# Kernel tuning notes

Measured on AMD Instinct MI355X. Metric: run time of the kernel, lower is better.

## Reference

```python
import jax, jax.numpy as jnp
import numpy as np


def _flip(x, c):
    # reflection about index c along the last (W) axis: out[..., i] = x[..., (c - i) mod W]
    W = x.shape[-1]
    idx = (c - jnp.arange(W)) % W
    return x[..., idx]


def setup_inputs() -> dict:
    key = jax.random.key(0)
    k1, k2, k3 = jax.random.split(key, 3)
    B, C, H, W = 8, 32, 256, 256
    x = jax.random.normal(k1, (B, C, H, W), dtype=jnp.float32)
    s = jax.random.normal(k2, (B, 11), dtype=jnp.float32)
    w = jax.random.uniform(k3, (B, 1, H, W), dtype=jnp.float32)
    w_param = jnp.ones((1,), dtype=jnp.float32)
    b_param = jnp.zeros((1,), dtype=jnp.float32)
    return {"x": x, "s": s, "w": w, "w_param": w_param, "b_param": b_param}


def reference(x, s, w, w_param, b_param):
    B, C, H, W = x.shape
    step = W // 8  # 32 for W=256
    # s -> sigmoid(w*s + b), shape [B, 11, 1, 1]
    sg = jax.nn.sigmoid(w_param * s + b_param).reshape(B, -1, 1, 1)
    # 7 circular shifts (45..315 deg) + 4 reflections
    a = w * x
    b = w
    for i in range(7):  # shifts step*1 .. step*7, gated by sg[:, 0..6]
        n = step * (i + 1)
        wk = sg[:, i:i + 1] * jnp.roll(w, n, axis=3)
        a = a + wk * jnp.roll(x, n, axis=3)
        b = b + wk
    for j in range(4):  # flips about step*1-1 .. step*4-1, gated by sg[:, 7..10]
        c = step * (j + 1) - 1
        wk = sg[:, 7 + j:8 + j] * _flip(w, c)
        a = a + wk * _flip(x, c)
        b = b + wk
    return a / b
```

## Files before the change

### kernel.cpp

```cpp
#include <hip/hip_runtime.h>
#include <math.h>

#define BB 8
#define CC 32
#define HH 256
#define WW 256
#define CHW (CC * HH * WW)
#define HW  (HH * WW)
#define NTERM 12
#define CH_PER_ITER 4

__global__ __launch_bounds__(256)
void symctrl2_kernel(const float* __restrict__ x,
                     const float* __restrict__ s,
                     const float* __restrict__ w,
                     const float* __restrict__ w_param,
                     const float* __restrict__ b_param,
                     float* __restrict__ out) {
    const int bh = blockIdx.x;
    const int b  = bh >> 8;
    const int h  = bh & (HH - 1);
    const int i  = threadIdx.x;

    __shared__ float w_row[WW];
    __shared__ float sg[11];
    __shared__ float x_lds[CH_PER_ITER][WW];

    const float* wrow_g = w + ((size_t)b * HH + h) * WW;
    w_row[i] = wrow_g[i];

    if (i < 11) {
        float v = w_param[0] * s[b * 11 + i] + b_param[0];
        sg[i] = 1.0f / (1.0f + expf(-v));
    }
    __syncthreads();

    int   src[NTERM];
    float gw[NTERM];
    src[0] = i;
    gw[0]  = w_row[i];
    #pragma unroll
    for (int k = 1; k <= 7; ++k) {
        int sidx = (i - 32 * k) & (WW - 1);
        src[k] = sidx;
        gw[k]  = sg[k - 1] * w_row[sidx];
    }
    #pragma unroll
    for (int j = 0; j < 4; ++j) {
        int c    = 32 * (j + 1) - 1;
        int sidx = (c - i) & (WW - 1);
        src[8 + j] = sidx;
        gw[8 + j]  = sg[7 + j] * w_row[sidx];
    }
    float den = 0.0f;
    #pragma unroll
    for (int k = 0; k < NTERM; ++k) den += gw[k];
    const float rden = 1.0f / den;

    const float* xb = x   + (size_t)b * CHW + (size_t)h * WW;
    float*       ob = out + (size_t)b * CHW + (size_t)h * WW;

    const int cc = threadIdx.x >> 6;
    const int p4 = (threadIdx.x & 63) << 2;

    for (int c0 = 0; c0 < CC; c0 += CH_PER_ITER) {
        const float4 v = *reinterpret_cast<const float4*>(
            xb + (size_t)(c0 + cc) * HW + p4);
        *reinterpret_cast<float4*>(&x_lds[cc][p4]) = v;
        __syncthreads();

        #pragma unroll
        for (int c = 0; c < CH_PER_ITER; ++c) {
            float num = 0.0f;
            #pragma unroll
            for (int k = 0; k < NTERM; ++k)
                num = fmaf(gw[k], x_lds[c][src[k]], num);
            ob[(size_t)(c0 + c) * HW + i] = num * rden;
        }
        __syncthreads();
    }
}

extern "C" void kernel_launch(void* const* d_in, const int* in_sizes, int n_in,
                              void* d_out, int out_size, void* d_ws, size_t ws_size,
                              hipStream_t stream) {
    const float* x  = (const float*)d_in[0];
    const float* s  = (const float*)d_in[1];
    const float* w  = (const float*)d_in[2];
    const float* wp = (const float*)d_in[3];
    const float* bp = (const float*)d_in[4];
    float* out = (float*)d_out;

    dim3 grid(BB * HH);
    dim3 block(WW);
    symctrl2_kernel<<<grid, block, 0, stream>>>(x, s, w, wp, bp, out);
}
```

Before: 122.5 us.

## Vectorize per-wave channel processing with float4 LDS, prefetch, and no barriers

Each wavefront now owns every fourth channel and keeps its own double-buffered LDS rows, so the block-wide __syncthreads calls go away. Each thread computes four adjacent output pixels using float4 global loads, float4 LDS reads and float4 stores; the reflection terms read a contiguous reversed window. Weights are loaded as float4 directly from global memory, with the gate and the reciprocal denominator folded into them once. The next channel's row is prefetched into registers while the current one is computed. The cost is higher register use (48 weight registers plus 12 indices), which matters against the occupancy hint of 4 blocks in the launch bounds.

```diff
diff --git a/kernel.cpp b/kernel.cpp
--- a/kernel.cpp
+++ b/kernel.cpp
@@ -5,79 +5,93 @@
 #define CC 32
 #define HH 256
 #define WW 256
-#define CHW (CC * HH * WW)
-#define HW  (HH * WW)
-#define NTERM 12
-#define CH_PER_ITER 4
+#define HW_ (HH * WW)
+#define CHW_ (CC * HW_)
 
-__global__ __launch_bounds__(256)
+__global__ __launch_bounds__(256, 4)
 void symctrl2_kernel(const float* __restrict__ x,
                      const float* __restrict__ s,
-                     const float* __restrict__ w,
+                     const float* __restrict__ wg,
                      const float* __restrict__ w_param,
                      const float* __restrict__ b_param,
                      float* __restrict__ out) {
     const int bh = blockIdx.x;
     const int b  = bh >> 8;
     const int h  = bh & (HH - 1);
-    const int i  = threadIdx.x;
+    const int wv = threadIdx.x >> 6;
+    const int l  = threadIdx.x & 63;
+    const int p0 = l << 2;
 
-    __shared__ float w_row[WW];
-    __shared__ float sg[11];
-    __shared__ float x_lds[CH_PER_ITER][WW];
+    __shared__ __align__(16) float x_lds[4][2][WW];
+    __shared__ float sg_lds[4][16];
 
-    const float* wrow_g = w + ((size_t)b * HH + h) * WW;
-    w_row[i] = wrow_g[i];
+    if (l < 11) {
+        float v = w_param[0] * s[b * 11 + l] + b_param[0];
+        sg_lds[wv][l] = 1.0f / (1.0f + expf(-v));
+    }
 
-    if (i < 11) {
-        float v = w_param[0] * s[b * 11 + i] + b_param[0];
-        sg[i] = 1.0f / (1.0f + expf(-v));
+    int srcb[12];
+    srcb[0] = p0;
+    #pragma unroll
+    for (int k = 1; k <= 7; ++k)
+        srcb[k] = (p0 - 32 * k) & (WW - 1);
+    #pragma unroll
+    for (int j = 0; j < 4; ++j)
+        srcb[8 + j] = (32 * j + 28 - p0) & (WW - 1);
+
+    const float* wrow = wg + ((size_t)b * HH + h) * WW;
+    float wr[12][4];
+    float den0 = 0.f, den1 = 0.f, den2 = 0.f, den3 = 0.f;
+    #pragma unroll
+    for (int t = 0; t < 12; ++t) {
+        const float4 w4 = *reinterpret_cast<const float4*>(wrow + srcb[t]);
+        const float gt = (t == 0) ? 1.0f : sg_lds[wv][t - 1];
+        if (t < 8) {
+            wr[t][0] = gt * w4.x; wr[t][1] = gt * w4.y;
+            wr[t][2] = gt * w4.z; wr[t][3] = gt * w4.w;
+        } else {
+            wr[t][0] = gt * w4.w; wr[t][1] = gt * w4.z;
+            wr[t][2] = gt * w4.y; wr[t][3] = gt * w4.x;
+        }
+        den0 += wr[t][0]; den1 += wr[t][1]; den2 += wr[t][2]; den3 += wr[t][3];
     }
-    __syncthreads();
+    const float r0 = 1.0f / den0, r1 = 1.0f / den1,
+                r2 = 1.0f / den2, r3 = 1.0f / den3;
+    #pragma unroll
+    for (int t = 0; t < 12; ++t) {
+        wr[t][0] *= r0; wr[t][1] *= r1; wr[t][2] *= r2; wr[t][3] *= r3;
+    }
 
-    int   src[NTERM];
-    float gw[NTERM];
-    src[0] = i;
-    gw[0]  = w_row[i];
+    const float* xb = x   + (size_t)b * CHW_ + (size_t)h * WW + (size_t)wv * HW_;
+    float*       ob = out + (size_t)b * CHW_ + (size_t)h * WW + (size_t)wv * HW_;
+
+    float4 nxt = *reinterpret_cast<const float4*>(xb + p0);
     #pragma unroll
-    for (int k = 1; k <= 7; ++k) {
-        int sidx = (i - 32 * k) & (WW - 1);
-        src[k] = sidx;
-        gw[k]  = sg[k - 1] * w_row[sidx];
-    }
-    #pragma unroll
-    for (int j = 0; j < 4; ++j) {
-        int c    = 32 * (j + 1) - 1;
-        int sidx = (c - i) & (WW - 1);
-        src[8 + j] = sidx;
-        gw[8 + j]  = sg[7 + j] * w_row[sidx];
-    }
-    float den = 0.0f;
-    #pragma unroll
-    for (int k = 0; k < NTERM; ++k) den += gw[k];
-    const float rden = 1.0f / den;
+    for (int it = 0; it < 8; ++it) {
+        float* row = x_lds[wv][it & 1];
+        *reinterpret_cast<float4*>(row + p0) = nxt;
+        if (it < 7)
+            nxt = *reinterpret_cast<const float4*>(
+                xb + (size_t)(it + 1) * (4 * HW_) + p0);
 
-    const float* xb = x   + (size_t)b * CHW + (size_t)h * WW;
-    float*       ob = out + (size_t)b * CHW + (size_t)h * WW;
-
-    const int cc = threadIdx.x >> 6;
-    const int p4 = (threadIdx.x & 63) << 2;
-
-    for (int c0 = 0; c0 < CC; c0 += CH_PER_ITER) {
-        const float4 v = *reinterpret_cast<const float4*>(
-            xb + (size_t)(c0 + cc) * HW + p4);
-        *reinterpret_cast<float4*>(&x_lds[cc][p4]) = v;
-        __syncthreads();
-
+        float a0 = 0.f, a1 = 0.f, a2 = 0.f, a3 = 0.f;
         #pragma unroll
-        for (int c = 0; c < CH_PER_ITER; ++c) {
-            float num = 0.0f;
-            #pragma unroll
-            for (int k = 0; k < NTERM; ++k)
-                num = fmaf(gw[k], x_lds[c][src[k]], num);
-            ob[(size_t)(c0 + c) * HW + i] = num * rden;
+        for (int t = 0; t < 12; ++t) {
+            const float4 xq = *reinterpret_cast<const float4*>(row + srcb[t]);
+            if (t < 8) {
+                a0 = fmaf(wr[t][0], xq.x, a0);
+                a1 = fmaf(wr[t][1], xq.y, a1);
+                a2 = fmaf(wr[t][2], xq.z, a2);
+                a3 = fmaf(wr[t][3], xq.w, a3);
+            } else {
+                a0 = fmaf(wr[t][0], xq.w, a0);
+                a1 = fmaf(wr[t][1], xq.z, a1);
+                a2 = fmaf(wr[t][2], xq.y, a2);
+                a3 = fmaf(wr[t][3], xq.x, a3);
+            }
         }
-        __syncthreads();
+        float4 o4 = make_float4(a0, a1, a2, a3);
+        *reinterpret_cast<float4*>(ob + (size_t)it * (4 * HW_) + p0) = o4;
     }
 }
 
@@ -89,9 +103,9 @@
     const float* w  = (const float*)d_in[2];
     const float* wp = (const float*)d_in[3];
     const float* bp = (const float*)d_in[4];
-    float* out = (float*)d_out;
+    float* outp = (float*)d_out;
 
     dim3 grid(BB * HH);
-    dim3 block(WW);
-    symctrl2_kernel<<<grid, block, 0, stream>>>(x, s, w, wp, bp, out);
+    dim3 block(256);
+    symctrl2_kernel<<<grid, block, 0, stream>>>(x, s, w, wp, bp, outp);
 }
```

Result: slower. 127.5 us (+4.1%).

## Register-resident row processing with DPP half-row mirror instead of LDS gathers

Applied to the files above, without the earlier changes.

Each 8-lane group now owns one full 256-wide row of one channel, holding w and x as eight float4 registers per lane. Circular shifts by 32 become register index rotations and reflections become a DPP row half-mirror, so the LDS staging, per-element gathers and block barriers are gone. The cost is much higher register pressure: 32-element den, num and P arrays per lane, with a launch bound requesting 2 blocks per SM. The denominator and sigmoid gates are also recomputed per thread, and division now uses the fast reciprocal.

```diff
diff --git a/kernel.cpp b/kernel.cpp
--- a/kernel.cpp
+++ b/kernel.cpp
@@ -5,79 +5,136 @@
 #define CC 32
 #define HH 256
 #define WW 256
-#define CHW (CC * HH * WW)
-#define HW  (HH * WW)
-#define NTERM 12
-#define CH_PER_ITER 4
 
-__global__ __launch_bounds__(256)
+__device__ __forceinline__ float half_mirror(float v) {
+    int i = __builtin_bit_cast(int, v);
+    i = __builtin_amdgcn_update_dpp(i, i, 0x141, 0xf, 0xf, true);
+    return __builtin_bit_cast(float, i);
+}
+
+__global__ __launch_bounds__(256, 2)
 void symctrl2_kernel(const float* __restrict__ x,
                      const float* __restrict__ s,
-                     const float* __restrict__ w,
+                     const float* __restrict__ wg,
                      const float* __restrict__ w_param,
                      const float* __restrict__ b_param,
                      float* __restrict__ out) {
-    const int bh = blockIdx.x;
-    const int b  = bh >> 8;
-    const int h  = bh & (HH - 1);
-    const int i  = threadIdx.x;
+    const int bh  = blockIdx.x;
+    const int b   = bh >> 8;
+    const int h   = bh & (HH - 1);
+    const int wv  = threadIdx.x >> 6;
+    const int l   = threadIdx.x & 63;
+    const int row = l >> 3;
+    const int u   = l & 7;
+    const int c   = (wv << 3) + row;
 
-    __shared__ float w_row[WW];
-    __shared__ float sg[11];
-    __shared__ float x_lds[CH_PER_ITER][WW];
+    const float* wrow = wg  + ((size_t)b * HH + h) * WW;
+    const float* xrow = x   + (((size_t)b * CC + c) * HH + h) * WW;
+    float*       orow = out + (((size_t)b * CC + c) * HH + h) * WW;
 
-    const float* wrow_g = w + ((size_t)b * HH + h) * WW;
-    w_row[i] = wrow_g[i];
+    float4 wq[8], xq[8];
+    #pragma unroll
+    for (int q = 0; q < 8; ++q)
+        wq[q] = *reinterpret_cast<const float4*>(wrow + 32 * q + 4 * u);
+    #pragma unroll
+    for (int q = 0; q < 8; ++q)
+        xq[q] = *reinterpret_cast<const float4*>(xrow + 32 * q + 4 * u);
 
-    if (i < 11) {
-        float v = w_param[0] * s[b * 11 + i] + b_param[0];
-        sg[i] = 1.0f / (1.0f + expf(-v));
-    }
-    __syncthreads();
-
-    int   src[NTERM];
-    float gw[NTERM];
-    src[0] = i;
-    gw[0]  = w_row[i];
+    const float wp = w_param[0], bpv = b_param[0];
+    float gk[8], gf[4];
+    gk[0] = 1.0f;
     #pragma unroll
-    for (int k = 1; k <= 7; ++k) {
-        int sidx = (i - 32 * k) & (WW - 1);
-        src[k] = sidx;
-        gw[k]  = sg[k - 1] * w_row[sidx];
+    for (int k = 0; k < 7; ++k) {
+        float v = wp * s[b * 11 + k] + bpv;
+        gk[k + 1] = 1.0f / (1.0f + __expf(-v));
     }
     #pragma unroll
     for (int j = 0; j < 4; ++j) {
-        int c    = 32 * (j + 1) - 1;
-        int sidx = (c - i) & (WW - 1);
-        src[8 + j] = sidx;
-        gw[8 + j]  = sg[7 + j] * w_row[sidx];
+        float v = wp * s[b * 11 + 7 + j] + bpv;
+        gf[j] = 1.0f / (1.0f + __expf(-v));
     }
-    float den = 0.0f;
+
+    float den[8][4];
     #pragma unroll
-    for (int k = 0; k < NTERM; ++k) den += gw[k];
-    const float rden = 1.0f / den;
+    for (int g = 0; g < 8; ++g) {
+        float d0 = 0.f, d1 = 0.f, d2 = 0.f, d3 = 0.f;
+        #pragma unroll
+        for (int k = 0; k < 8; ++k) {
+            const float4 w4 = wq[(g - k) & 7];
+            d0 = fmaf(gk[k], w4.x, d0);
+            d1 = fmaf(gk[k], w4.y, d1);
+            d2 = fmaf(gk[k], w4.z, d2);
+            d3 = fmaf(gk[k], w4.w, d3);
+        }
+        den[g][0] = d0; den[g][1] = d1; den[g][2] = d2; den[g][3] = d3;
+    }
+    #pragma unroll
+    for (int q = 0; q < 8; ++q) {
+        const float m0 = half_mirror(wq[q].x);
+        const float m1 = half_mirror(wq[q].y);
+        const float m2 = half_mirror(wq[q].z);
+        const float m3 = half_mirror(wq[q].w);
+        #pragma unroll
+        for (int j = 0; j < 4; ++j) {
+            const int g = (j - q) & 7;
+            den[g][0] = fmaf(gf[j], m3, den[g][0]);
+            den[g][1] = fmaf(gf[j], m2, den[g][1]);
+            den[g][2] = fmaf(gf[j], m1, den[g][2]);
+            den[g][3] = fmaf(gf[j], m0, den[g][3]);
+        }
+    }
+    float rden[8][4];
+    #pragma unroll
+    for (int g = 0; g < 8; ++g)
+        #pragma unroll
+        for (int e = 0; e < 4; ++e)
+            rden[g][e] = __builtin_amdgcn_rcpf(den[g][e]);
 
-    const float* xb = x   + (size_t)b * CHW + (size_t)h * WW;
-    float*       ob = out + (size_t)b * CHW + (size_t)h * WW;
-
-    const int cc = threadIdx.x >> 6;
-    const int p4 = (threadIdx.x & 63) << 2;
-
-    for (int c0 = 0; c0 < CC; c0 += CH_PER_ITER) {
-        const float4 v = *reinterpret_cast<const float4*>(
-            xb + (size_t)(c0 + cc) * HW + p4);
-        *reinterpret_cast<float4*>(&x_lds[cc][p4]) = v;
-        __syncthreads();
-
+    float P[8][4];
+    #pragma unroll
+    for (int q = 0; q < 8; ++q) {
+        P[q][0] = wq[q].x * xq[q].x;
+        P[q][1] = wq[q].y * xq[q].y;
+        P[q][2] = wq[q].z * xq[q].z;
+        P[q][3] = wq[q].w * xq[q].w;
+    }
+    float num[8][4];
+    #pragma unroll
+    for (int g = 0; g < 8; ++g) {
+        float n0 = 0.f, n1 = 0.f, n2 = 0.f, n3 = 0.f;
         #pragma unroll
-        for (int c = 0; c < CH_PER_ITER; ++c) {
-            float num = 0.0f;
-            #pragma unroll
-            for (int k = 0; k < NTERM; ++k)
-                num = fmaf(gw[k], x_lds[c][src[k]], num);
-            ob[(size_t)(c0 + c) * HW + i] = num * rden;
+        for (int k = 0; k < 8; ++k) {
+            const int q = (g - k) & 7;
+            n0 = fmaf(gk[k], P[q][0], n0);
+            n1 = fmaf(gk[k], P[q][1], n1);
+            n2 = fmaf(gk[k], P[q][2], n2);
+            n3 = fmaf(gk[k], P[q][3], n3);
         }
-        __syncthreads();
+        num[g][0] = n0; num[g][1] = n1; num[g][2] = n2; num[g][3] = n3;
+    }
+    #pragma unroll
+    for (int q = 0; q < 8; ++q) {
+        const float m0 = half_mirror(P[q][0]);
+        const float m1 = half_mirror(P[q][1]);
+        const float m2 = half_mirror(P[q][2]);
+        const float m3 = half_mirror(P[q][3]);
+        #pragma unroll
+        for (int j = 0; j < 4; ++j) {
+            const int g = (j - q) & 7;
+            num[g][0] = fmaf(gf[j], m3, num[g][0]);
+            num[g][1] = fmaf(gf[j], m2, num[g][1]);
+            num[g][2] = fmaf(gf[j], m1, num[g][2]);
+            num[g][3] = fmaf(gf[j], m0, num[g][3]);
+        }
+    }
+    #pragma unroll
+    for (int g = 0; g < 8; ++g) {
+        float4 o;
+        o.x = num[g][0] * rden[g][0];
+        o.y = num[g][1] * rden[g][1];
+        o.z = num[g][2] * rden[g][2];
+        o.w = num[g][3] * rden[g][3];
+        *reinterpret_cast<float4*>(orow + 32 * g + 4 * u) = o;
     }
 }
 
@@ -89,9 +146,9 @@
     const float* w  = (const float*)d_in[2];
     const float* wp = (const float*)d_in[3];
     const float* bp = (const float*)d_in[4];
-    float* out = (float*)d_out;
+    float* outp = (float*)d_out;
 
     dim3 grid(BB * HH);
-    dim3 block(WW);
-    symctrl2_kernel<<<grid, block, 0, stream>>>(x, s, w, wp, bp, out);
+    dim3 block(256);
+    symctrl2_kernel<<<grid, block, 0, stream>>>(x, s, w, wp, bp, outp);
 }
```

Result: faster. 120.0 us (-2.0%).
